# Kernel tuning notes

Hardware: AMD Instinct MI355X
Metric: run time of the kernel (lower is better)

## Reference

```python
import jax, jax.numpy as jnp
import numpy as np

B, P, C = 128, 8732, 21          # batch, num_priors (SSD300), num_classes incl. background
TOP_K = 200
VAR0, VAR1 = 0.1, 0.2            # SSD prior variances
CONF_THRESH = 0.01
NMS_THRESH = 0.45


def setup_inputs() -> dict:
    key = jax.random.key(0)
    k1, k2, k3, k4 = jax.random.split(key, 4)
    loc_data = jax.random.normal(k1, (B, P, 4), jnp.float32)
    conf_data = jax.random.normal(k2, (B * P, C), jnp.float32)
    # priors: (cx, cy, w, h) in [0,1], positive widths/heights
    cxy = jax.random.uniform(k3, (P, 2), jnp.float32)
    wh = jax.random.uniform(k4, (P, 2), jnp.float32, minval=0.02, maxval=0.3)
    prior_data = jnp.concatenate([cxy, wh], axis=-1)
    return {"loc_data": loc_data, "conf_data": conf_data, "prior_data": prior_data}


def _decode(loc, priors):
    # loc: [B,P,4], priors: [P,4] (cx,cy,w,h) -> corner boxes [B,P,4]
    xy = priors[:, :2] + loc[..., :2] * VAR0 * priors[:, 2:]
    wh = priors[:, 2:] * jnp.exp(loc[..., 2:] * VAR1)
    return jnp.concatenate([xy - wh * 0.5, xy + wh * 0.5], axis=-1)


def _nms_single(boxes, scores, idxs):
    # boxes [P,4] corners, scores [P] (-1 where below conf_thresh), idxs [P] int class ids
    x1, y1, x2, y2 = boxes[:, 0], boxes[:, 1], boxes[:, 2], boxes[:, 3]
    areas = (x2 - x1) * (y2 - y1)

    def body(s, _):
        i = jnp.argmax(s)          # highest remaining score
        si = s[i]
        valid = si > 0.0
        bi = boxes[i]
        # IoU of bi against all boxes
        ix1 = jnp.maximum(bi[0], x1)
        iy1 = jnp.maximum(bi[1], y1)
        ix2 = jnp.minimum(bi[2], x2)
        iy2 = jnp.minimum(bi[3], y2)
        inter = jnp.maximum(ix2 - ix1, 0.0) * jnp.maximum(iy2 - iy1, 0.0)
        area_i = (bi[2] - bi[0]) * (bi[3] - bi[1])
        iou = inter / (area_i + areas - inter)
        # class-aware (batched) NMS: only suppress same-class boxes; also kills i itself (iou=1)
        suppress = (iou > NMS_THRESH) & (idxs == idxs[i])
        s_new = jnp.where(suppress, -1.0, s)
        row = jnp.where(
            valid,
            jnp.concatenate([bi, si[None], idxs[i].astype(jnp.float32)[None]]),
            jnp.zeros(6, dtype=boxes.dtype),
        )
        return s_new, row

    _, rows = jax.lax.scan(body, scores, None, length=TOP_K)
    return rows  # [TOP_K, 6] = (x1,y1,x2,y2,score,class)


def reference(loc_data, conf_data, prior_data):
    # softmax over classes, drop background, per-prior best fg class
    conf = jax.nn.softmax(conf_data, axis=-1)[:, 1:].reshape(B, P, C - 1)
    scores = conf.max(axis=-1)           # [B,P]
    cls = jnp.argmax(conf, axis=-1)      # [B,P] fg class id (0..C-2)
    boxes = _decode(loc_data, prior_data)  # [B,P,4]
    masked = jnp.where(scores > CONF_THRESH, scores, -1.0)
    return jax.vmap(_nms_single)(boxes, masked, cls)  # [B, TOP_K, 6]
```

## Files before the change

### kernel.cpp

```cpp
#include <hip/hip_runtime.h>


typedef unsigned long long u64;

#define BATCH 128
#define NPRIOR 8732
#define NCLS 21
#define TOPK 200
#define T 1024
#define TARGET 256
#define CAP 384
#define NBIN 4096
#define KW 6
#define NCHUNK 9

__device__ __forceinline__ double exp_fast(double x) {
  const double LOG2E = 1.4426950408889634;
  const double LN2_HI = 6.93147180369123816490e-01;
  const double LN2_LO = 1.90821492927058770002e-10;
  double n = rint(x * LOG2E);
  double r = fma(-n, LN2_HI, x);
  r = fma(-n, LN2_LO, r);
  double p = 2.505210838544172e-08;
  p = fma(p, r, 2.755731922398589e-07);
  p = fma(p, r, 2.7557319223985893e-06);
  p = fma(p, r, 2.48015873015873e-05);
  p = fma(p, r, 1.984126984126984e-04);
  p = fma(p, r, 1.388888888888889e-03);
  p = fma(p, r, 8.333333333333333e-03);
  p = fma(p, r, 4.1666666666666664e-02);
  p = fma(p, r, 1.6666666666666666e-01);
  p = fma(p, r, 0.5);
  p = fma(p, r, 1.0);
  p = fma(p, r, 1.0);
  double scale = __longlong_as_double(((long long)(1023 + (int)n)) << 52);
  return p * scale;
}

__device__ __forceinline__ void radix_cut(const int* hist, int tid, int tcap,
                                          int* wtot, int* cut) {
  if (tid == 0) cut[2] = 0;
  const int base = tid * 4;
  const int cs = hist[base] + hist[base + 1] + hist[base + 2] + hist[base + 3];
  const int lane = tid & 63;
  int suf = cs;
#pragma unroll
  for (int off = 1; off < 64; off <<= 1) {
    int v = __shfl_down(suf, off);
    if (lane + off < 64) suf += v;
  }
  if (lane == 0) wtot[tid >> 6] = suf;
  __syncthreads();
  if (tid < 16) {
    int v = wtot[tid];
    int s = v;
#pragma unroll
    for (int off = 1; off < 16; off <<= 1) {
      int o = __shfl_down(s, off);
      if (tid + off < 16) s += o;
    }
    if (tid == 0) wtot[16] = s;
    wtot[tid] = s - v;
  }
  __syncthreads();
  const int total = wtot[16];
  if (total > 0) {
    const int target = total < tcap ? total : tcap;
    const int S = suf + wtot[tid >> 6];
    const int Snext = S - cs;
    if (S >= target && Snext < target) {
      int acc = Snext;
      for (int bn = base + 3; bn >= base; --bn) {
        acc += hist[bn];
        if (acc >= target) {
          cut[0] = bn; cut[1] = acc - hist[bn]; cut[2] = acc;
          break;
        }
      }
    }
  }
  __syncthreads();
}

__global__ __launch_bounds__(T) void detect_kernel(
    const float* __restrict__ loc, const float* __restrict__ conf,
    const float* __restrict__ prior, float* __restrict__ out) {
  __shared__ __align__(16) float srow[T * NCLS];
  __shared__ int hist[NBIN];
  __shared__ u64 buf[CAP];
  __shared__ u64 ebuf[CAP];
  __shared__ u64 buf2[CAP];
  __shared__ float4 cbox[CAP];
  __shared__ float car[CAP];
  __shared__ int ccl[CAP];
  __shared__ u64 KILL[CAP * KW];
  __shared__ int wtot[17];
  __shared__ int cut1[3], cut2[3];
  __shared__ u64 Ash[KW], KFsh[KW], ACCsh[KW];
  __shared__ float4 abox[TOPK];
  __shared__ float aar[TOPK];
  __shared__ int acl[TOPK];
  __shared__ int sh_cnt, sh_nA;

  const int tid = threadIdx.x;
  const int b = blockIdx.x;
  const float* confb = conf + (long long)b * (NPRIOR * NCLS);
  const float4* loc4 = ((const float4*)loc) + (long long)b * NPRIOR;
  const float4* pr4 = (const float4*)prior;
  float* outb = out + (long long)b * (TOPK * 6);

  u64 kreg[NCHUNK];
#pragma unroll
  for (int c = 0; c < NCHUNK; ++c) {
    const int r0 = c * T;
    const int nrows = (r0 + T <= NPRIOR) ? T : (NPRIOR - r0);
    const int nf4 = (nrows * NCLS) >> 2;
    const float4* src = (const float4*)(confb + (long long)r0 * NCLS);
    float4* dst = (float4*)srow;
    for (int k = tid; k < nf4; k += T) dst[k] = src[k];
    __syncthreads();
    u64 key = 0ULL;
    if (tid < nrows) {
      const float* row = srow + tid * NCLS;
      float m = row[0];
#pragma unroll
      for (int j = 1; j < NCLS; ++j) m = fmaxf(m, row[j]);
      float sum = __expf(row[0] - m);
      float bestr = row[1];
      float beste = __expf(row[1] - m);
      sum += beste;
      int bi = 1;
#pragma unroll
      for (int j = 2; j < NCLS; ++j) {
        float rv = row[j];
        float ej = __expf(rv - m);
        sum += ej;
        if (rv > bestr) { bestr = rv; bi = j; beste = ej; }
      }
      float score = __fdividef(beste, sum);
      const int p = r0 + tid;
      if (score > 0.01f) {
        key = ((u64)__float_as_uint(score) << 32) |
              ((u64)(16383 - p) << 10) | (u64)(bi - 1);
      }
    }
    kreg[c] = key;
    __syncthreads();
  }

  if (tid == 0) sh_nA = 0;

  u64 ub = ~0ULL;
  int Mr = 0, total = 0;
  while (true) {
    for (int i = tid; i < NBIN; i += T) hist[i] = 0;
    __syncthreads();
#pragma unroll
    for (int c = 0; c < NCHUNK; ++c) {
      u64 k = kreg[c];
      if (k && k < ub) atomicAdd(&hist[(int)((k >> 46) & 0xFFF)], 1);
    }
    __syncthreads();
    radix_cut(hist, tid, TARGET, wtot, cut1);
    total = wtot[16];
    int M = cut1[2];
    if (M == 0) break;
    const int c1 = cut1[0];
    const int baseA = cut1[1];
    const bool need2 = (M > CAP);
    int c2 = 0;
    if (need2) {
      for (int i = tid; i < NBIN; i += T) hist[i] = 0;
      __syncthreads();
#pragma unroll
      for (int c = 0; c < NCHUNK; ++c) {
        u64 k = kreg[c];
        if (k && k < ub && (int)((k >> 46) & 0xFFF) == c1)
          atomicAdd(&hist[(int)((k >> 34) & 0xFFF)], 1);
      }
      __syncthreads();
      const int tcap2 = (total < TARGET ? total : TARGET) - baseA;
      radix_cut(hist, tid, tcap2, wtot, cut2);
      c2 = cut2[0];
      M = baseA + cut2[2];
      if (M > CAP) {
        int Md = M - hist[c2];
        if (Md > 0) { M = Md; c2 = c2 + 1; } else { M = CAP; }
      }
    }
    if (tid == 0) sh_cnt = 0;
    const u64 ubold = ub;
    ub = need2 ? (((u64)c1 << 46) + ((u64)c2 << 34)) : ((u64)c1 << 46);
    __syncthreads();
#pragma unroll
    for (int c = 0; c < NCHUNK; ++c) {
      u64 k = kreg[c];
      bool psel = false;
      if (k && k < ubold) {
        int b1 = (int)((k >> 46) & 0xFFF);
        psel = need2 ? (b1 > c1 || (b1 == c1 && (int)((k >> 34) & 0xFFF) >= c2))
                     : (b1 >= c1);
      }
      u64 mask = __ballot(psel ? 1 : 0);
      if (mask) {
        int lane = tid & 63;
        int leader = __ffsll((unsigned long long)mask) - 1;
        int bpos = 0;
        if (lane == leader) bpos = atomicAdd(&sh_cnt, __popcll(mask));
        bpos = __shfl(bpos, leader);
        if (psel) {
          int pos = bpos + __popcll(mask & ((1ULL << lane) - 1ULL));
          if (pos < CAP) buf[pos] = k;
        }
      }
    }
    __syncthreads();
    Mr = sh_cnt;
    if (Mr > CAP) Mr = CAP;
    if (Mr == 0) break;

    float4 lreg = make_float4(0.f, 0.f, 0.f, 0.f);
    float4 preg = make_float4(0.f, 0.f, 0.f, 0.f);
    int myp = 0, mycl = 0;
    if (tid < Mr) {
      u64 ak = buf[tid];
      mycl = (int)(ak & 0x1FULL);
      myp = 16383 - (int)((ak >> 10) & 0x3FFFULL);
      lreg = loc4[myp];
      preg = pr4[myp];
      const float* crow = confb + (long long)myp * NCLS;
      float cr[NCLS];
#pragma unroll
      for (int j = 0; j < NCLS; ++j) cr[j] = crow[j];
      double m = (double)cr[0];
#pragma unroll
      for (int j = 1; j < NCLS; ++j) m = fmax(m, (double)cr[j]);
      double sum = 0.0, best = -1.0;
#pragma unroll
      for (int j = 0; j < NCLS; ++j) {
        double ej = exp_fast((double)cr[j] - m);
        sum += ej;
        if (j >= 1 && ej > best) best = ej;
      }
      double score = best / sum;
      u64 sb = (u64)__double_as_longlong(score);
      ebuf[tid] = ((sb >> 24) << 24) | ((u64)(16383 - myp) << 10) | (u64)mycl;
    }
    if (tid < KW) { Ash[tid] = 0ULL; KFsh[tid] = 0ULL; }
    __syncthreads();
    const int nA0 = sh_nA;

    if (tid < Mr) {
      u64 ka = ebuf[tid];
      int ra = 0;
      int i = 0;
      for (; i + 8 <= Mr; i += 8) {
        u64 k0 = ebuf[i], k1 = ebuf[i + 1], k2 = ebuf[i + 2], k3 = ebuf[i + 3];
        u64 k4 = ebuf[i + 4], k5 = ebuf[i + 5], k6 = ebuf[i + 6],
            k7 = ebuf[i + 7];
        ra += (int)(k0 > ka) + (int)(k1 > ka) + (int)(k2 > ka) +
              (int)(k3 > ka) + (int)(k4 > ka) + (int)(k5 > ka) +
              (int)(k6 > ka) + (int)(k7 > ka);
      }
      for (; i < Mr; ++i) ra += (int)(ebuf[i] > ka);
      buf2[ra] = ka;
      double cx = (double)preg.x + (double)lreg.x * 0.1 * (double)preg.z;
      double cy = (double)preg.y + (double)lreg.y * 0.1 * (double)preg.w;
      double w = (double)preg.z * exp_fast((double)lreg.z * 0.2);
      double h = (double)preg.w * exp_fast((double)lreg.w * 0.2);
      float x1 = (float)(cx - w * 0.5), y1 = (float)(cy - h * 0.5);
      float x2 = (float)(cx + w * 0.5), y2 = (float)(cy + h * 0.5);
      cbox[ra] = make_float4(x1, y1, x2, y2);
      car[ra] = (x2 - x1) * (y2 - y1);
      ccl[ra] = mycl;
    }
    __syncthreads();

    if (nA0 > 0 && tid < Mr) {
      const int t = tid;
      float4 my = cbox[t];
      float mar = car[t];
      int mcl = ccl[t];
      bool sup = false;
      for (int a = 0; a < nA0; ++a) {
        if (acl[a] == mcl) {
          float4 ab = abox[a];
          float ix1 = fmaxf(ab.x, my.x), iy1 = fmaxf(ab.y, my.y);
          float ix2 = fminf(ab.z, my.z), iy2 = fminf(ab.w, my.w);
          float inter = fmaxf(ix2 - ix1, 0.f) * fmaxf(iy2 - iy1, 0.f);
          if (inter > 0.45f * (aar[a] + mar - inter)) sup = true;
        }
      }
      if (sup) atomicOr(&Ash[t >> 6], 1ULL << (t & 63));
    }
    for (int idx = tid; idx < KW * 512; idx += T) {
      const int seg = idx >> 9;
      const int t = idx & 511;
      if (t < Mr) {
        const int i0 = seg * 64;
        int i1 = i0 + 64;
        if (i1 > Mr) i1 = Mr;
        u64 mm = 0ULL;
        if (i1 > t) {
          float4 my = cbox[t];
          float mar = car[t];
          int mcl = ccl[t];
          int is = (i0 > t + 1) ? i0 : (t + 1);
#pragma unroll 4
          for (int i = is; i < i1; ++i) {
            if (ccl[i] == mcl) {
              float4 cb = cbox[i];
              float ix1 = fmaxf(my.x, cb.x), iy1 = fmaxf(my.y, cb.y);
              float ix2 = fminf(my.z, cb.z), iy2 = fminf(my.w, cb.w);
              float inter = fmaxf(ix2 - ix1, 0.f) * fmaxf(iy2 - iy1, 0.f);
              if (inter > 0.45f * (mar + car[i] - inter))
                mm |= 1ULL << (i - i0);
            }
          }
        }
        KILL[t * KW + seg] = mm;
        if (mm) atomicOr(&KFsh[t >> 6], 1ULL << (t & 63));
      }
    }
    __syncthreads();
    if (tid < 64) {
      u64 A0, A1, A2, A3, A4, A5;
      {
        u64 v[KW];
#pragma unroll
        for (int w = 0; w < KW; ++w) {
          int rem = Mr - 64 * w;
          u64 vm =
              (rem >= 64) ? ~0ULL : (rem <= 0 ? 0ULL : ((1ULL << rem) - 1ULL));
          v[w] = vm & ~Ash[w];
        }
        A0 = v[0]; A1 = v[1]; A2 = v[2]; A3 = v[3]; A4 = v[4]; A5 = v[5];
      }
      u64 C0 = 0, C1 = 0, C2 = 0, C3 = 0, C4 = 0, C5 = 0;
      int nacc = nA0;
      bool full = false;
#define KILLUPD(cidx) do { const u64* kc = &KILL[(cidx) * KW];      \
      A0 &= ~kc[0]; A1 &= ~kc[1]; A2 &= ~kc[2];                     \
      A3 &= ~kc[3]; A4 &= ~kc[4]; A5 &= ~kc[5]; } while (0)
#define RESW(w, Aw, Cw) if (!full) {                                \
      const u64 KFw = KFsh[w];                                      \
      int lim = Mr - (w) * 64; if (lim > 64) lim = 64;              \
      for (int q = 0; q < lim; ++q) {                               \
        if ((Aw >> q) & 1ULL) {                                     \
          Cw |= 1ULL << q; ++nacc;                                  \
          if (nacc == TOPK) { full = true; break; }                 \
          if ((KFw >> q) & 1ULL) KILLUPD((w) * 64 + q);             \
        } } }
      RESW(0, A0, C0)
      RESW(1, A1, C1)
      RESW(2, A2, C2)
      RESW(3, A3, C3)
      RESW(4, A4, C4)
      RESW(5, A5, C5)
#undef RESW
#undef KILLUPD
      if (tid == 0) {
        ACCsh[0] = C0; ACCsh[1] = C1; ACCsh[2] = C2;
        ACCsh[3] = C3; ACCsh[4] = C4; ACCsh[5] = C5;
        sh_nA = nacc;
      }
    }
    __syncthreads();
    if (tid < Mr) {
      const int t = tid;
      const int w = t >> 6, q = t & 63;
      const u64 accw = ACCsh[w];
      if ((accw >> q) & 1ULL) {
        int rank = nA0;
#pragma unroll
        for (int w2 = 0; w2 < KW; ++w2)
          if (w2 < w) rank += __popcll(ACCsh[w2]);
        rank += __popcll(accw & ((q == 0) ? 0ULL : ((1ULL << q) - 1ULL)));
        float4 bx = cbox[t];
        float sc =
            (float)__longlong_as_double((long long)((buf2[t] >> 24) << 24));
        float* o = outb + rank * 6;
        o[0] = bx.x; o[1] = bx.y; o[2] = bx.z; o[3] = bx.w;
        o[4] = sc; o[5] = (float)ccl[t];
        abox[rank] = bx; aar[rank] = car[t]; acl[rank] = ccl[t];
      }
    }
    __syncthreads();
    if (sh_nA >= TOPK) break;
    if (total - Mr <= 0) break;
  }
  __syncthreads();
  const int nAf = sh_nA;
  for (int i = nAf * 6 + tid; i < TOPK * 6; i += T) outb[i] = 0.0f;
}

extern "C" void kernel_launch(void* const* d_in, const int* in_sizes, int n_in,
                              void* d_out, int out_size, void* d_ws,
                              size_t ws_size, hipStream_t stream) {
  const float* loc = (const float*)d_in[0];
  const float* conf = (const float*)d_in[1];
  const float* prior = (const float*)d_in[2];
  float* out = (float*)d_out;
  (void)d_ws; (void)ws_size;

  detect_kernel<<<BATCH, T, 0, stream>>>(loc, conf, prior, out);
}
```

Before: 228.7 us.

## Split softmax/score key generation into a separate fully-parallel prep kernel

Moves the per-prior softmax, best-class and key packing out of the 128-block NMS kernel into a separate kernel over all rows, launched with many 256-thread blocks. The keys go through workspace memory and the NMS kernel reads them directly. This spreads the bandwidth-heavy conf pass across the whole GPU instead of 128 workgroups, and drops the large shared staging buffer. The cost is a second launch and an extra global round-trip of 8-byte keys. Each thread also reads its 21 floats with strided, uncoalesced loads.

Result: faster. 204.9 us (-10.4%).

```diff
diff --git a/kernel.cpp b/kernel.cpp
--- a/kernel.cpp
+++ b/kernel.cpp
@@ -37,6 +37,39 @@
   return p * scale;
 }
 
+__global__ __launch_bounds__(256) void prep_kernel(
+    const float* __restrict__ conf, u64* __restrict__ keys) {
+  const int r = blockIdx.x * 256 + threadIdx.x;
+  const float* __restrict__ rp = conf + (long long)r * NCLS;
+  float cr[NCLS];
+#pragma unroll
+  for (int j = 0; j < NCLS; ++j) cr[j] = rp[j];
+  float m = cr[0];
+#pragma unroll
+  for (int j = 1; j < NCLS; ++j) m = fmaxf(m, cr[j]);
+  float sum = __expf(cr[0] - m);
+  float bestr = cr[1];
+  float beste = __expf(cr[1] - m);
+  sum += beste;
+  int bi = 1;
+#pragma unroll
+  for (int j = 2; j < NCLS; ++j) {
+    float rv = cr[j];
+    float ej = __expf(rv - m);
+    sum += ej;
+    if (rv > bestr) { bestr = rv; bi = j; beste = ej; }
+  }
+  float score = __fdividef(beste, sum);
+
+  const int p = r % NPRIOR;
+  u64 key = 0ULL;
+  if (score > 0.01f) {
+    key = ((u64)__float_as_uint(score) << 32) |
+          ((u64)(16383 - p) << 10) | (u64)(bi - 1);
+  }
+  keys[r] = key;
+}
+
 __device__ __forceinline__ void radix_cut(const int* hist, int tid, int tcap,
                                           int* wtot, int* cut) {
   if (tid == 0) cut[2] = 0;
@@ -82,10 +115,10 @@
   __syncthreads();
 }
 
-__global__ __launch_bounds__(T) void detect_kernel(
+__global__ __launch_bounds__(T) void selnms_kernel(
     const float* __restrict__ loc, const float* __restrict__ conf,
-    const float* __restrict__ prior, float* __restrict__ out) {
-  __shared__ __align__(16) float srow[T * NCLS];
+    const float* __restrict__ prior, const u64* __restrict__ keys,
+    float* __restrict__ out) {
   __shared__ int hist[NBIN];
   __shared__ u64 buf[CAP];
   __shared__ u64 ebuf[CAP];
@@ -108,46 +141,14 @@
   const float4* loc4 = ((const float4*)loc) + (long long)b * NPRIOR;
   const float4* pr4 = (const float4*)prior;
   float* outb = out + (long long)b * (TOPK * 6);
+  const u64* kb = keys + (long long)b * NPRIOR;
 
   u64 kreg[NCHUNK];
 #pragma unroll
   for (int c = 0; c < NCHUNK; ++c) {
-    const int r0 = c * T;
-    const int nrows = (r0 + T <= NPRIOR) ? T : (NPRIOR - r0);
-    const int nf4 = (nrows * NCLS) >> 2;
-    const float4* src = (const float4*)(confb + (long long)r0 * NCLS);
-    float4* dst = (float4*)srow;
-    for (int k = tid; k < nf4; k += T) dst[k] = src[k];
-    __syncthreads();
-    u64 key = 0ULL;
-    if (tid < nrows) {
-      const float* row = srow + tid * NCLS;
-      float m = row[0];
-#pragma unroll
-      for (int j = 1; j < NCLS; ++j) m = fmaxf(m, row[j]);
-      float sum = __expf(row[0] - m);
-      float bestr = row[1];
-      float beste = __expf(row[1] - m);
-      sum += beste;
-      int bi = 1;
-#pragma unroll
-      for (int j = 2; j < NCLS; ++j) {
-        float rv = row[j];
-        float ej = __expf(rv - m);
-        sum += ej;
-        if (rv > bestr) { bestr = rv; bi = j; beste = ej; }
-      }
-      float score = __fdividef(beste, sum);
-      const int p = r0 + tid;
-      if (score > 0.01f) {
-        key = ((u64)__float_as_uint(score) << 32) |
-              ((u64)(16383 - p) << 10) | (u64)(bi - 1);
-      }
-    }
-    kreg[c] = key;
-    __syncthreads();
-  }
-
+    const int i = c * T + tid;
+    kreg[c] = (i < NPRIOR) ? kb[i] : 0ULL;
+  }
   if (tid == 0) sh_nA = 0;
 
   u64 ub = ~0ULL;
@@ -401,7 +402,10 @@
   const float* conf = (const float*)d_in[1];
   const float* prior = (const float*)d_in[2];
   float* out = (float*)d_out;
-  (void)d_ws; (void)ws_size;
-
-  detect_kernel<<<BATCH, T, 0, stream>>>(loc, conf, prior, out);
+
+  u64* keys = (u64*)d_ws;
+  const int nrows_blocks = (BATCH * NPRIOR) / 256;
+
+  prep_kernel<<<nrows_blocks, 256, 0, stream>>>(conf, keys);
+  selnms_kernel<<<BATCH, T, 0, stream>>>(loc, conf, prior, keys, out);
 }
```
